# Performance work log

Hardware: AMD Instinct MI355X
Metric: run time of the kernel (lower is better)

The kernel has to match this reference:

```python
import jax, jax.numpy as jnp
import numpy as np

LMBDA = {"rec": 1.0, "bpp": 1.0}


def setup_inputs() -> dict:
    key = jax.random.key(0)
    k1, k2, k3 = jax.random.split(key, 3)
    B, P, D = 8, 4096, 3
    x_hat = jax.random.normal(k1, (B, P, D), dtype=jnp.float32)
    pos = jax.random.normal(k2, (B, P, D), dtype=jnp.float32)
    # latent likelihoods in (0, 1], CompressAI-style [B, C, L]
    likelihoods = jax.random.uniform(k3, (B, 192, 1024), dtype=jnp.float32,
                                     minval=1e-6, maxval=1.0)
    return {"x_hat": x_hat, "pos": pos, "likelihoods": likelihoods}


def chamfer_distance(x, y):
    # x: [B, P, 3], y: [B, Q, 3]; squared-distance chamfer, mean over points,
    # summed both directions, averaged over batch (pytorch3d default 'mean').
    x2 = jnp.sum(x * x, axis=-1)                       # [B, P]
    y2 = jnp.sum(y * y, axis=-1)                       # [B, Q]
    xy = jnp.einsum("bpd,bqd->bpq", x, y)              # [B, P, Q]
    d2 = x2[:, :, None] + y2[:, None, :] - 2.0 * xy    # [B, P, Q]
    d2 = jnp.maximum(d2, 0.0)
    cham_x = jnp.mean(jnp.min(d2, axis=2), axis=1)     # [B] x -> y NN
    cham_y = jnp.mean(jnp.min(d2, axis=1), axis=1)     # [B] y -> x NN
    return jnp.mean(cham_x + cham_y)


def reference(x_hat, pos, likelihoods):
    B, P, _ = pos.shape
    # rate loss: bits per point over the whole batch
    num_points = B * P
    bpp_loss = jnp.sum(-jnp.log2(likelihoods)) / num_points
    # reconstruction loss: bidirectional chamfer distance
    rec_loss = chamfer_distance(x_hat, pos)
    loss = LMBDA["rec"] * rec_loss + LMBDA["bpp"] * bpp_loss
    return loss, bpp_loss, rec_loss
```

## Files before the change

### kernel.cpp

```cpp
#include <hip/hip_runtime.h>
#include <math.h>

#define BATCH   8
#define NPTS    4096
#define THREADS 512
#define WAVES   8
#define ROWS_PB 128
#define CHUNK   1024
#define NSTEP   2
#define NBLOCKS 512
#define NBPP    512

#define LIK_PER_BLK 768

typedef __attribute__((ext_vector_type(8)))  __bf16 bf16x8;
typedef __attribute__((ext_vector_type(16))) float  f32x16;

__device__ inline bf16x8 packFeat(float f0, float f1, float f2, float f3, float f4) {
    bf16x8 r;
    r[0] = (__bf16)f0; r[1] = (__bf16)f1; r[2] = (__bf16)f2;
    r[3] = (__bf16)f3; r[4] = (__bf16)f4;
    r[5] = (__bf16)0.0f; r[6] = (__bf16)0.0f; r[7] = (__bf16)0.0f;
    return r;
}

__device__ inline bf16x8 colFeat(float y0, float y1, float y2) {
    return packFeat(-2.f * y0, -2.f * y1, -2.f * y2, 1.0f,
                    fmaf(y0, y0, fmaf(y1, y1, y2 * y2)));
}

__global__ __launch_bounds__(THREADS, 4) void fused_kernel(
    const float* __restrict__ Xin, const float* __restrict__ Yin,
    const float* __restrict__ lik,
    float* __restrict__ recPartial, float* __restrict__ bppPartial)
{
    const float* X; const float* Y;
    if (blockIdx.z == 0) { X = Xin; Y = Yin; }
    else                 { X = Yin; Y = Xin; }

    const int b = blockIdx.y;
    const int rowBase = (int)blockIdx.x * ROWS_PB;
    const int blk = ((int)blockIdx.z * gridDim.y + blockIdx.y) * gridDim.x + blockIdx.x;

    const int tid  = threadIdx.x;
    const int lane = tid & 63;
    const int w    = tid >> 6;
    const int rg   = w >> 1;
    const int ph   = w & 1;
    const int li   = lane & 31;
    const int hi   = lane >> 5;

    __shared__ bf16x8 yfeat[2][2 * CHUNK];
    __shared__ float  cmb[2][ROWS_PB];
    __shared__ float  wr[WAVES], wb[WAVES];

    float bs = 0.0f;
    {
        const float4* l4 = (const float4*)lik + (size_t)blk * LIK_PER_BLK;
        for (int i = tid; i < LIK_PER_BLK; i += THREADS) {
            float4 v = l4[i];
            bs -= __log2f(v.x * v.y * v.z * v.w);
        }
    }

    bf16x8 a;
    {
        const float* p = X + ((size_t)b * NPTS + rowBase + rg * 32 + li) * 3;
        float x0 = p[0], x1 = p[1], x2 = p[2];
        a = packFeat(x0, x1, x2, fmaf(x0, x0, fmaf(x1, x1, x2 * x2)), 1.0f);
    }

    f32x16 m, kZero;
    #pragma unroll
    for (int j = 0; j < 16; ++j) { m[j] = 3.0e38f; kZero[j] = 0.0f; }

    const size_t yb0 = (size_t)b * NPTS;

    {
        const float* p0 = Y + (yb0 + tid) * 3;
        const float* p1 = Y + (yb0 + 512 + tid) * 3;
        const float* p2 = Y + (yb0 + 2048 + tid) * 3;
        const float* p3 = Y + (yb0 + 2560 + tid) * 3;
        yfeat[0][tid]               = colFeat(p0[0], p0[1], p0[2]);
        yfeat[0][tid + 512]         = colFeat(p1[0], p1[1], p1[2]);
        yfeat[0][CHUNK + tid]       = colFeat(p2[0], p2[1], p2[2]);
        yfeat[0][CHUNK + 512 + tid] = colFeat(p3[0], p3[1], p3[2]);
    }
    __syncthreads();

    int buf = 0;
    for (int s = 0; s < NSTEP; ++s) {
        float u0,u1,u2, v0,v1,v2, t0,t1,t2, q0,q1,q2;
        if (s + 1 < NSTEP) {
            const float* p0 = Y + (yb0 + (s + 1) * CHUNK + tid) * 3;
            const float* p1 = p0 + 512 * 3;
            const float* p2 = Y + (yb0 + 2048 + (s + 1) * CHUNK + tid) * 3;
            const float* p3 = p2 + 512 * 3;
            u0 = p0[0]; u1 = p0[1]; u2 = p0[2];
            v0 = p1[0]; v1 = p1[1]; v2 = p1[2];
            t0 = p2[0]; t1 = p2[1]; t2 = p2[2];
            q0 = p3[0]; q1 = p3[1]; q2 = p3[2];
        }

        const bf16x8* yb = &yfeat[buf][ph * CHUNK];
        #pragma unroll 2
        for (int f = 0; f < 32; f += 2) {
            bf16x8 bA = yb[f * 32 + li];
            bf16x8 bB = yb[(f + 1) * 32 + li];
            f32x16 d = __builtin_amdgcn_mfma_f32_32x32x16_bf16(a, bA, kZero, 0, 0, 0);
            f32x16 e = __builtin_amdgcn_mfma_f32_32x32x16_bf16(a, bB, kZero, 0, 0, 0);
            #pragma unroll
            for (int j = 0; j < 16; ++j)
                m[j] = fminf(fminf(d[j], e[j]), m[j]);
        }

        if (s + 1 < NSTEP) {
            yfeat[buf ^ 1][tid]               = colFeat(u0, u1, u2);
            yfeat[buf ^ 1][tid + 512]         = colFeat(v0, v1, v2);
            yfeat[buf ^ 1][CHUNK + tid]       = colFeat(t0, t1, t2);
            yfeat[buf ^ 1][CHUNK + 512 + tid] = colFeat(q0, q1, q2);
        }
        __syncthreads();
        buf ^= 1;
    }

    #pragma unroll
    for (int mask = 1; mask <= 16; mask <<= 1)
        #pragma unroll
        for (int j = 0; j < 16; ++j)
            m[j] = fminf(m[j], __shfl_xor(m[j], mask, 64));

    if (li == 0) {
        #pragma unroll
        for (int j = 0; j < 16; ++j) {
            int ri = (j & 3) + 8 * (j >> 2) + 4 * hi;
            cmb[ph][rg * 32 + ri] = m[j];
        }
    }

    #pragma unroll
    for (int off = 32; off >= 1; off >>= 1) bs += __shfl_down(bs, off, 64);
    if (lane == 0) wb[w] = bs;
    __syncthreads();

    float s = 0.0f;
    if (tid < ROWS_PB) {
        float mv = fminf(cmb[0][tid], cmb[1][tid]);
        s = fmaxf(0.5f * mv, 0.0f);
    }
    #pragma unroll
    for (int off = 32; off >= 1; off >>= 1) s += __shfl_down(s, off, 64);
    if (lane == 0) wr[w] = s;
    __syncthreads();
    if (tid == 0) {
        float rs = 0.0f, bbv = 0.0f;
        #pragma unroll
        for (int j = 0; j < WAVES; ++j) { rs += wr[j]; bbv += wb[j]; }
        recPartial[blk] = rs;
        bppPartial[blk] = bbv;
    }
}

__global__ __launch_bounds__(256) void final_kernel(const float* __restrict__ recPartial,
                                                    const float* __restrict__ bppPartial,
                                                    float* __restrict__ out) {
    float sr = 0.0f, sb = 0.0f;
    for (int i = threadIdx.x; i < NBLOCKS; i += 256) sr += recPartial[i];
    for (int i = threadIdx.x; i < NBPP;    i += 256) sb += bppPartial[i];
    #pragma unroll
    for (int off = 32; off >= 1; off >>= 1) {
        sr += __shfl_down(sr, off, 64);
        sb += __shfl_down(sb, off, 64);
    }
    __shared__ float wrf[4], wbf[4];
    int lane = threadIdx.x & 63, w = threadIdx.x >> 6;
    if (lane == 0) { wrf[w] = sr; wbf[w] = sb; }
    __syncthreads();
    if (threadIdx.x == 0) {
        float rec = (wrf[0] + wrf[1] + wrf[2] + wrf[3]) * (1.0f / 32768.0f);
        float bpp = (wbf[0] + wbf[1] + wbf[2] + wbf[3]) * (1.0f / 32768.0f);
        out[0] = rec + bpp;
        out[1] = bpp;
        out[2] = rec;
    }
}

extern "C" void kernel_launch(void* const* d_in, const int* in_sizes, int n_in,
                              void* d_out, int out_size, void* d_ws, size_t ws_size,
                              hipStream_t stream) {
    const float* x_hat = (const float*)d_in[0];
    const float* pos   = (const float*)d_in[1];
    const float* lik   = (const float*)d_in[2];
    float* out = (float*)d_out;

    float* recPartial = (float*)d_ws;
    float* bppPartial = recPartial + NBLOCKS;

    dim3 grid(NPTS / ROWS_PB, BATCH, 2);
    fused_kernel<<<grid, THREADS, 0, stream>>>(x_hat, pos, lik, recPartial, bppPartial);
    final_kernel<<<1, 256, 0, stream>>>(recPartial, bppPartial, out);
}
```

Before: 20.42 us.

## Give each wave two row tiles and split columns four ways for B-fragment reuse

Each wave now owns 64 rows (two A fragments) and a quarter of every column chunk, instead of 32 rows and half a chunk. Each column fragment read from LDS now feeds two MFMAs, which halves LDS read traffic per MFMA. The cost is a second accumulator set (more VGPRs), twice the shuffle reduction work per wave, and a four-way combine in shared memory at the end.

```diff
diff --git a/kernel.cpp b/kernel.cpp
--- a/kernel.cpp
+++ b/kernel.cpp
@@ -6,8 +6,9 @@
 #define THREADS 512
 #define WAVES   8
 #define ROWS_PB 128
-#define CHUNK   1024
+#define SCHUNK  2048
 #define NSTEP   2
+#define QCOLS   512
 #define NBLOCKS 512
 #define NBPP    512
 
@@ -45,13 +46,13 @@
     const int tid  = threadIdx.x;
     const int lane = tid & 63;
     const int w    = tid >> 6;
-    const int rg   = w >> 1;
-    const int ph   = w & 1;
+    const int rg   = w >> 2;
+    const int qh   = w & 3;
     const int li   = lane & 31;
     const int hi   = lane >> 5;
 
-    __shared__ bf16x8 yfeat[2][2 * CHUNK];
-    __shared__ float  cmb[2][ROWS_PB];
+    __shared__ bf16x8 yfeat[2][SCHUNK];
+    __shared__ float  cmb[4][ROWS_PB];
     __shared__ float  wr[WAVES], wb[WAVES];
 
     float bs = 0.0f;
@@ -63,28 +64,28 @@
         }
     }
 
-    bf16x8 a;
+    bf16x8 a0, a1;
     {
-        const float* p = X + ((size_t)b * NPTS + rowBase + rg * 32 + li) * 3;
+        const float* p = X + ((size_t)b * NPTS + rowBase + rg * 64 + li) * 3;
         float x0 = p[0], x1 = p[1], x2 = p[2];
-        a = packFeat(x0, x1, x2, fmaf(x0, x0, fmaf(x1, x1, x2 * x2)), 1.0f);
-    }
-
-    f32x16 m, kZero;
-    #pragma unroll
-    for (int j = 0; j < 16; ++j) { m[j] = 3.0e38f; kZero[j] = 0.0f; }
+        a0 = packFeat(x0, x1, x2, fmaf(x0, x0, fmaf(x1, x1, x2 * x2)), 1.0f);
+        const float* q = p + 32 * 3;
+        float z0 = q[0], z1 = q[1], z2 = q[2];
+        a1 = packFeat(z0, z1, z2, fmaf(z0, z0, fmaf(z1, z1, z2 * z2)), 1.0f);
+    }
+
+    f32x16 m0, m1, kZero;
+    #pragma unroll
+    for (int j = 0; j < 16; ++j) { m0[j] = 3.0e38f; m1[j] = 3.0e38f; kZero[j] = 0.0f; }
 
     const size_t yb0 = (size_t)b * NPTS;
 
     {
-        const float* p0 = Y + (yb0 + tid) * 3;
-        const float* p1 = Y + (yb0 + 512 + tid) * 3;
-        const float* p2 = Y + (yb0 + 2048 + tid) * 3;
-        const float* p3 = Y + (yb0 + 2560 + tid) * 3;
-        yfeat[0][tid]               = colFeat(p0[0], p0[1], p0[2]);
-        yfeat[0][tid + 512]         = colFeat(p1[0], p1[1], p1[2]);
-        yfeat[0][CHUNK + tid]       = colFeat(p2[0], p2[1], p2[2]);
-        yfeat[0][CHUNK + 512 + tid] = colFeat(p3[0], p3[1], p3[2]);
+        #pragma unroll
+        for (int i = 0; i < 4; ++i) {
+            const float* p = Y + (yb0 + i * 512 + tid) * 3;
+            yfeat[0][i * 512 + tid] = colFeat(p[0], p[1], p[2]);
+        }
     }
     __syncthreads();
 
@@ -92,49 +93,58 @@
     for (int s = 0; s < NSTEP; ++s) {
         float u0,u1,u2, v0,v1,v2, t0,t1,t2, q0,q1,q2;
         if (s + 1 < NSTEP) {
-            const float* p0 = Y + (yb0 + (s + 1) * CHUNK + tid) * 3;
+            const float* p0 = Y + (yb0 + SCHUNK + tid) * 3;
             const float* p1 = p0 + 512 * 3;
-            const float* p2 = Y + (yb0 + 2048 + (s + 1) * CHUNK + tid) * 3;
-            const float* p3 = p2 + 512 * 3;
+            const float* p2 = p0 + 1024 * 3;
+            const float* p3 = p0 + 1536 * 3;
             u0 = p0[0]; u1 = p0[1]; u2 = p0[2];
             v0 = p1[0]; v1 = p1[1]; v2 = p1[2];
             t0 = p2[0]; t1 = p2[1]; t2 = p2[2];
             q0 = p3[0]; q1 = p3[1]; q2 = p3[2];
         }
 
-        const bf16x8* yb = &yfeat[buf][ph * CHUNK];
+        const bf16x8* yb = &yfeat[buf][qh * QCOLS];
         #pragma unroll 2
-        for (int f = 0; f < 32; f += 2) {
+        for (int f = 0; f < 16; f += 2) {
             bf16x8 bA = yb[f * 32 + li];
             bf16x8 bB = yb[(f + 1) * 32 + li];
-            f32x16 d = __builtin_amdgcn_mfma_f32_32x32x16_bf16(a, bA, kZero, 0, 0, 0);
-            f32x16 e = __builtin_amdgcn_mfma_f32_32x32x16_bf16(a, bB, kZero, 0, 0, 0);
+            f32x16 d = __builtin_amdgcn_mfma_f32_32x32x16_bf16(a0, bA, kZero, 0, 0, 0);
+            f32x16 e = __builtin_amdgcn_mfma_f32_32x32x16_bf16(a0, bB, kZero, 0, 0, 0);
             #pragma unroll
             for (int j = 0; j < 16; ++j)
-                m[j] = fminf(fminf(d[j], e[j]), m[j]);
+                m0[j] = fminf(fminf(d[j], e[j]), m0[j]);
+            d = __builtin_amdgcn_mfma_f32_32x32x16_bf16(a1, bA, kZero, 0, 0, 0);
+            e = __builtin_amdgcn_mfma_f32_32x32x16_bf16(a1, bB, kZero, 0, 0, 0);
+            #pragma unroll
+            for (int j = 0; j < 16; ++j)
+                m1[j] = fminf(fminf(d[j], e[j]), m1[j]);
         }
 
         if (s + 1 < NSTEP) {
-            yfeat[buf ^ 1][tid]               = colFeat(u0, u1, u2);
-            yfeat[buf ^ 1][tid + 512]         = colFeat(v0, v1, v2);
-            yfeat[buf ^ 1][CHUNK + tid]       = colFeat(t0, t1, t2);
-            yfeat[buf ^ 1][CHUNK + 512 + tid] = colFeat(q0, q1, q2);
+            yfeat[buf ^ 1][tid]        = colFeat(u0, u1, u2);
+            yfeat[buf ^ 1][tid +  512] = colFeat(v0, v1, v2);
+            yfeat[buf ^ 1][tid + 1024] = colFeat(t0, t1, t2);
+            yfeat[buf ^ 1][tid + 1536] = colFeat(q0, q1, q2);
         }
         __syncthreads();
         buf ^= 1;
     }
 
     #pragma unroll
-    for (int mask = 1; mask <= 16; mask <<= 1)
-        #pragma unroll
-        for (int j = 0; j < 16; ++j)
-            m[j] = fminf(m[j], __shfl_xor(m[j], mask, 64));
+    for (int mask = 1; mask <= 16; mask <<= 1) {
+        #pragma unroll
+        for (int j = 0; j < 16; ++j) {
+            m0[j] = fminf(m0[j], __shfl_xor(m0[j], mask, 64));
+            m1[j] = fminf(m1[j], __shfl_xor(m1[j], mask, 64));
+        }
+    }
 
     if (li == 0) {
         #pragma unroll
         for (int j = 0; j < 16; ++j) {
             int ri = (j & 3) + 8 * (j >> 2) + 4 * hi;
-            cmb[ph][rg * 32 + ri] = m[j];
+            cmb[qh][rg * 64 + ri]      = m0[j];
+            cmb[qh][rg * 64 + 32 + ri] = m1[j];
         }
     }
 
@@ -145,7 +155,8 @@
 
     float s = 0.0f;
     if (tid < ROWS_PB) {
-        float mv = fminf(cmb[0][tid], cmb[1][tid]);
+        float mv = fminf(fminf(cmb[0][tid], cmb[1][tid]),
+                         fminf(cmb[2][tid], cmb[3][tid]));
         s = fmaxf(0.5f * mv, 0.0f);
     }
     #pragma unroll
```

New measurement: 31.29 us. +53.2%, slower.
